# Kernel tuning notes

Measured on AMD Instinct MI355X. Metric: run time of the kernel, lower is better.

Reference implementation:

```python
import jax, jax.numpy as jnp
import numpy as np

B, S = 4096, 8192

def setup_inputs() -> dict:
    key = jax.random.key(0)
    k1, k2, k3 = jax.random.split(key, 3)
    scores = jax.random.normal(k1, (B, S, 1), dtype=jnp.float32)
    label = jax.random.randint(k2, (B,), 0, 2).astype(jnp.float32)
    # seqlen in [16, 8192) so k = seqlen//16 + 1 is always <= seqlen
    seqlen = jax.random.randint(k3, (B,), 16, S, dtype=jnp.int32)
    return {"scores": scores, "label": label, "seqlen": seqlen}


def reference(scores, label, seqlen):
    # scores: [B, S, 1] -> [B, S]; per-row variable-length top-k mean (k = seqlen//16 + 1),
    # then sigmoid + BCE vs label. Vectorized via mask + descending sort + prefix mask.
    s = scores.squeeze(-1)                                   # [B, S]
    pos = jnp.arange(s.shape[1])                             # [S]
    valid = pos[None, :] < seqlen[:, None]                   # [B, S] ragged mask
    masked = jnp.where(valid, s, -jnp.inf)
    desc = -jnp.sort(-masked, axis=-1)                       # descending sort per row
    k = seqlen // 16 + 1                                     # _cfg.k == -1 branch
    topk_mask = pos[None, :] < k[:, None]                    # first k sorted entries
    topk_mean = jnp.sum(jnp.where(topk_mask, desc, 0.0), axis=-1) / k.astype(s.dtype)
    inst = jax.nn.sigmoid(topk_mean)                         # [B]
    # nn.BCELoss (mean reduction)
    eps = 1e-12
    loss = -jnp.mean(label * jnp.log(inst + eps) + (1.0 - label) * jnp.log(1.0 - inst + eps))
    return loss
```

## Files before the change

kernel.cpp:

```cpp
#include <hip/hip_runtime.h>
#include <stdint.h>


#define SLEN 8192
#define BLK 256
#define NWAVE (BLK / 64)
#define VPT (SLEN / BLK / 4)
#define NB 256
#define CAP 1024
#define LOV (-6.0f)
#define SCALE (NB / 12.0f)

__device__ __forceinline__ int bin_of(float x) {
  float t = (x - LOV) * SCALE;
  int b = (int)t;
  b = b < 0 ? 0 : (b > NB - 1 ? NB - 1 : b);
  return b;
}

__global__ __launch_bounds__(BLK, 8) void topk_bce_rows(
    const float* __restrict__ scores, const float* __restrict__ label,
    const int* __restrict__ seqlen, float* __restrict__ rowterm) {
  __shared__ uint32_t hist[NB];
  __shared__ float cand[CAP];
  __shared__ uint32_t wtot[NWAVE];
  __shared__ uint32_t selBin, selAbove;
  __shared__ int ccount;
  __shared__ float redbuf[NWAVE];

  const int row = blockIdx.x;
  const int tid = threadIdx.x;
  const int lane = tid & 63;
  const int wave = tid >> 6;
  const int n = seqlen[row];
  const uint32_t k = (uint32_t)(n >> 4) + 1;

  const float4* src = reinterpret_cast<const float4*>(scores + (size_t)row * SLEN);
  float v[VPT * 4];
  #pragma unroll
  for (int i = 0; i < VPT; ++i) {
    int q4 = i * BLK + tid;
    if (4 * q4 < n) {
      float4 q = src[q4];
      v[i * 4 + 0] = q.x; v[i * 4 + 1] = q.y;
      v[i * 4 + 2] = q.z; v[i * 4 + 3] = q.w;
    }
  }

  hist[tid] = 0u;
  if (tid == 0) ccount = 0;
  __syncthreads();

  #pragma unroll
  for (int i = 0; i < VPT; ++i) {
    #pragma unroll
    for (int c = 0; c < 4; ++c) {
      int pos = i * (BLK * 4) + tid * 4 + c;
      if (pos < n) atomicAdd(&hist[bin_of(v[i * 4 + c])], 1u);
    }
  }
  __syncthreads();

  const uint32_t wsum = hist[tid];
  uint32_t sfx = wsum;
  #pragma unroll
  for (int d = 1; d < 64; d <<= 1) {
    uint32_t o = __shfl_down(sfx, d, 64);
    if (lane + d < 64) sfx += o;
  }
  if (lane == 0) wtot[wave] = sfx;
  __syncthreads();
  uint32_t tailw = 0;
  #pragma unroll
  for (int w = 0; w < NWAVE; ++w)
    if (w > wave) tailw += wtot[w];
  const uint32_t F = sfx + tailw;
  const uint32_t above = F - wsum;
  if (F >= k && above < k) { selBin = (uint32_t)tid; selAbove = above; }
  __syncthreads();
  const int bstar = (int)selBin;
  const uint32_t remaining = k - selAbove;

  float psum = 0.0f;
  #pragma unroll
  for (int i = 0; i < VPT; ++i) {
    #pragma unroll
    for (int c = 0; c < 4; ++c) {
      int pos = i * (BLK * 4) + tid * 4 + c;
      if (pos < n) {
        float x = v[i * 4 + c];
        int b = bin_of(x);
        if (b > bstar) {
          psum += x;
        } else if (b == bstar) {
          int idx = atomicAdd(&ccount, 1);
          if (idx < CAP) cand[idx] = x;
        }
      }
    }
  }
  __syncthreads();
  const int C = min(ccount, CAP);

  for (int i = tid; i < C; i += BLK) {
    float x = cand[i];
    uint32_t r = 0;
    for (int j = 0; j < C; ++j) {
      float y = cand[j];
      r += (uint32_t)((y > x) || (y == x && j < i));
    }
    if (r < remaining) psum += x;
  }

  #pragma unroll
  for (int d = 32; d >= 1; d >>= 1) psum += __shfl_down(psum, d, 64);
  if (lane == 0) redbuf[wave] = psum;
  __syncthreads();
  if (tid == 0) {
    float tot = 0.0f;
    #pragma unroll
    for (int w = 0; w < NWAVE; ++w) tot += redbuf[w];
    float mean = tot / (float)k;
    float inst = 1.0f / (1.0f + expf(-mean));
    float lab = label[row];
    float term = lab * logf(inst + 1e-12f) +
                 (1.0f - lab) * logf(1.0f - inst + 1e-12f);
    rowterm[row] = term;
  }
}

__global__ __launch_bounds__(1024) void reduce_rows(
    const float* __restrict__ rowterm, float* __restrict__ out, int rows) {
  __shared__ float red[16];
  const int tid = threadIdx.x;
  const int lane = tid & 63;
  const int wave = tid >> 6;
  float s = 0.0f;
  for (int i = tid; i < rows; i += 1024) s += rowterm[i];
  #pragma unroll
  for (int d = 32; d >= 1; d >>= 1) s += __shfl_down(s, d, 64);
  if (lane == 0) red[wave] = s;
  __syncthreads();
  if (tid == 0) {
    float tot = 0.0f;
    #pragma unroll
    for (int w = 0; w < 16; ++w) tot += red[w];
    out[0] = -tot / (float)rows;
  }
}

extern "C" void kernel_launch(void* const* d_in, const int* in_sizes, int n_in,
                              void* d_out, int out_size, void* d_ws, size_t ws_size,
                              hipStream_t stream) {
  const float* scores = (const float*)d_in[0];
  const float* label  = (const float*)d_in[1];
  const int*   seqlen = (const int*)d_in[2];
  float* out = (float*)d_out;
  float* rowterm = (float*)d_ws;

  const int rows = in_sizes[1];

  topk_bce_rows<<<rows, BLK, 0, stream>>>(scores, label, seqlen, rowterm);
  reduce_rows<<<1, 1024, 0, stream>>>(rowterm, out, rows);
}
```

Before: 186.5 us.

## Prefilter top-k candidates with a Gaussian-quantile threshold, exact fallback otherwise

Each row estimates a threshold from an inverse normal tail approximation with a safety margin. It then reads the row once, keeping only elements above that threshold in shared memory and histogramming only those. The bin selection and rank refinement run over this small candidate set instead of every element, which cuts the per-element histogram atomics and the second pass over the data. Dropping the register array of all row values also lowers register pressure. If the candidate count falls below k or overflows the buffer, the old exact three-pass path runs instead, at the cost of extra global reads for such rows.

```diff
diff --git a/kernel.cpp b/kernel.cpp
--- a/kernel.cpp
+++ b/kernel.cpp
@@ -5,24 +5,28 @@
 #define SLEN 8192
 #define BLK 256
 #define NWAVE (BLK / 64)
-#define VPT (SLEN / BLK / 4)
 #define NB 256
-#define CAP 1024
+#define CAP 2048
 #define LOV (-6.0f)
 #define SCALE (NB / 12.0f)
 
 __device__ __forceinline__ int bin_of(float x) {
-  float t = (x - LOV) * SCALE;
-  int b = (int)t;
-  b = b < 0 ? 0 : (b > NB - 1 ? NB - 1 : b);
-  return b;
+  int b = (int)((x - LOV) * SCALE);
+  return b < 0 ? 0 : (b > NB - 1 ? NB - 1 : b);
+}
+
+__device__ __forceinline__ float inv_q(float p) {
+  float t = sqrtf(-2.0f * logf(p));
+  return t - (2.30753f + 0.27061f * t) /
+                 (1.0f + 0.99229f * t + 0.04481f * t * t) -
+         0.03f;
 }
 
 __global__ __launch_bounds__(BLK, 8) void topk_bce_rows(
     const float* __restrict__ scores, const float* __restrict__ label,
     const int* __restrict__ seqlen, float* __restrict__ rowterm) {
+  __shared__ float cand[CAP];
   __shared__ uint32_t hist[NB];
-  __shared__ float cand[CAP];
   __shared__ uint32_t wtot[NWAVE];
   __shared__ uint32_t selBin, selAbove;
   __shared__ int ccount;
@@ -35,81 +39,139 @@
   const int n = seqlen[row];
   const uint32_t k = (uint32_t)(n >> 4) + 1;
 
+  const float sk = sqrtf((float)k);
+  const float p0 = ((float)k + 8.0f * sk + 16.0f) / (float)n;
+  const float t0 = (p0 >= 0.45f) ? -12.0f : inv_q(p0);
+
+  hist[tid] = 0u;
+  if (tid == 0) ccount = 0;
+  __syncthreads();
+
   const float4* src = reinterpret_cast<const float4*>(scores + (size_t)row * SLEN);
-  float v[VPT * 4];
   #pragma unroll
-  for (int i = 0; i < VPT; ++i) {
+  for (int i = 0; i < SLEN / 4 / BLK; ++i) {
     int q4 = i * BLK + tid;
     if (4 * q4 < n) {
       float4 q = src[q4];
-      v[i * 4 + 0] = q.x; v[i * 4 + 1] = q.y;
-      v[i * 4 + 2] = q.z; v[i * 4 + 3] = q.w;
-    }
-  }
-
-  hist[tid] = 0u;
-  if (tid == 0) ccount = 0;
-  __syncthreads();
-
-  #pragma unroll
-  for (int i = 0; i < VPT; ++i) {
-    #pragma unroll
-    for (int c = 0; c < 4; ++c) {
-      int pos = i * (BLK * 4) + tid * 4 + c;
-      if (pos < n) atomicAdd(&hist[bin_of(v[i * 4 + c])], 1u);
-    }
-  }
-  __syncthreads();
-
-  const uint32_t wsum = hist[tid];
-  uint32_t sfx = wsum;
-  #pragma unroll
-  for (int d = 1; d < 64; d <<= 1) {
-    uint32_t o = __shfl_down(sfx, d, 64);
-    if (lane + d < 64) sfx += o;
-  }
-  if (lane == 0) wtot[wave] = sfx;
-  __syncthreads();
-  uint32_t tailw = 0;
-  #pragma unroll
-  for (int w = 0; w < NWAVE; ++w)
-    if (w > wave) tailw += wtot[w];
-  const uint32_t F = sfx + tailw;
-  const uint32_t above = F - wsum;
-  if (F >= k && above < k) { selBin = (uint32_t)tid; selAbove = above; }
-  __syncthreads();
-  const int bstar = (int)selBin;
-  const uint32_t remaining = k - selAbove;
-
+      float xs[4] = {q.x, q.y, q.z, q.w};
+      #pragma unroll
+      for (int c = 0; c < 4; ++c) {
+        if (4 * q4 + c < n && xs[c] >= t0) {
+          int idx = atomicAdd(&ccount, 1);
+          if (idx < CAP) cand[idx] = xs[c];
+          atomicAdd(&hist[bin_of(xs[c])], 1u);
+        }
+      }
+    }
+  }
+  __syncthreads();
+
+  const int C0 = ccount;
   float psum = 0.0f;
-  #pragma unroll
-  for (int i = 0; i < VPT; ++i) {
-    #pragma unroll
-    for (int c = 0; c < 4; ++c) {
-      int pos = i * (BLK * 4) + tid * 4 + c;
-      if (pos < n) {
-        float x = v[i * 4 + c];
-        int b = bin_of(x);
-        if (b > bstar) {
-          psum += x;
-        } else if (b == bstar) {
-          int idx = atomicAdd(&ccount, 1);
-          if (idx < CAP) cand[idx] = x;
+
+  if (C0 >= (int)k && C0 <= CAP) {
+    const uint32_t wsum = hist[tid];
+    uint32_t sfx = wsum;
+    #pragma unroll
+    for (int d = 1; d < 64; d <<= 1) {
+      uint32_t o = __shfl_down(sfx, d, 64);
+      if (lane + d < 64) sfx += o;
+    }
+    if (lane == 0) wtot[wave] = sfx;
+    __syncthreads();
+    uint32_t tailw = 0;
+    #pragma unroll
+    for (int w = 0; w < NWAVE; ++w)
+      if (w > wave) tailw += wtot[w];
+    const uint32_t F = sfx + tailw;
+    const uint32_t above = F - wsum;
+    if (F >= k && above < k) selBin = (uint32_t)tid;
+    __syncthreads();
+    const int bstar = (int)selBin;
+
+    for (int i = tid; i < C0; i += BLK) {
+      float x = cand[i];
+      int b = bin_of(x);
+      if (b > bstar) {
+        psum += x;
+      } else if (b == bstar) {
+        uint32_t r = 0;
+        for (int j = 0; j < C0; ++j) {
+          float y = cand[j];
+          r += (uint32_t)((y > x) || (y == x && j < i));
         }
-      }
-    }
-  }
-  __syncthreads();
-  const int C = min(ccount, CAP);
-
-  for (int i = tid; i < C; i += BLK) {
-    float x = cand[i];
-    uint32_t r = 0;
-    for (int j = 0; j < C; ++j) {
-      float y = cand[j];
-      r += (uint32_t)((y > x) || (y == x && j < i));
-    }
-    if (r < remaining) psum += x;
+        if (r < k) psum += x;
+      }
+    }
+  } else {
+    hist[tid] = 0u;
+    if (tid == 0) ccount = 0;
+    __syncthreads();
+    #pragma unroll
+    for (int i = 0; i < SLEN / 4 / BLK; ++i) {
+      int q4 = i * BLK + tid;
+      if (4 * q4 < n) {
+        float4 q = src[q4];
+        float xs[4] = {q.x, q.y, q.z, q.w};
+        #pragma unroll
+        for (int c = 0; c < 4; ++c)
+          if (4 * q4 + c < n) atomicAdd(&hist[bin_of(xs[c])], 1u);
+      }
+    }
+    __syncthreads();
+
+    const uint32_t wsum = hist[tid];
+    uint32_t sfx = wsum;
+    #pragma unroll
+    for (int d = 1; d < 64; d <<= 1) {
+      uint32_t o = __shfl_down(sfx, d, 64);
+      if (lane + d < 64) sfx += o;
+    }
+    if (lane == 0) wtot[wave] = sfx;
+    __syncthreads();
+    uint32_t tailw = 0;
+    #pragma unroll
+    for (int w = 0; w < NWAVE; ++w)
+      if (w > wave) tailw += wtot[w];
+    const uint32_t F = sfx + tailw;
+    const uint32_t above = F - wsum;
+    if (F >= k && above < k) { selBin = (uint32_t)tid; selAbove = above; }
+    __syncthreads();
+    const int bstar = (int)selBin;
+    const uint32_t remaining = k - selAbove;
+
+    #pragma unroll
+    for (int i = 0; i < SLEN / 4 / BLK; ++i) {
+      int q4 = i * BLK + tid;
+      if (4 * q4 < n) {
+        float4 q = src[q4];
+        float xs[4] = {q.x, q.y, q.z, q.w};
+        #pragma unroll
+        for (int c = 0; c < 4; ++c) {
+          if (4 * q4 + c < n) {
+            float x = xs[c];
+            int b = bin_of(x);
+            if (b > bstar) {
+              psum += x;
+            } else if (b == bstar) {
+              int idx = atomicAdd(&ccount, 1);
+              if (idx < CAP) cand[idx] = x;
+            }
+          }
+        }
+      }
+    }
+    __syncthreads();
+    const int C = min(ccount, CAP);
+    for (int i = tid; i < C; i += BLK) {
+      float x = cand[i];
+      uint32_t r = 0;
+      for (int j = 0; j < C; ++j) {
+        float y = cand[j];
+        r += (uint32_t)((y > x) || (y == x && j < i));
+      }
+      if (r < remaining) psum += x;
+    }
   }
 
   #pragma unroll
```

New measurement: 362.3 us. +94.3%, slower.
